# Kernel tuning notes

Hardware: AMD Instinct MI355X
Metric: run time of the kernel (lower is better)

Reference implementation:

```python
import jax, jax.numpy as jnp
import numpy as np

B, S, V, H = 256, 1024, 256, 256


def setup_inputs() -> dict:
    key = jax.random.key(0)
    ks = jax.random.split(key, 12)
    s = 1.0 / np.sqrt(H)
    def u(k, shape):
        return jax.random.uniform(k, shape, jnp.float32, -s, s)
    return {
        "x": jax.random.normal(ks[0], (B, S, V), jnp.float32),
        "w_ih0": u(ks[1], (4 * H, V)),
        "w_hh0": u(ks[2], (4 * H, H)),
        "b_ih0": u(ks[3], (4 * H,)),
        "b_hh0": u(ks[4], (4 * H,)),
        "w_ih1": u(ks[5], (4 * H, H)),
        "w_hh1": u(ks[6], (4 * H, H)),
        "b_ih1": u(ks[7], (4 * H,)),
        "b_hh1": u(ks[8], (4 * H,)),
        "fc_w": u(ks[9], (V, H)),
        "fc_b": u(ks[10], (V,)),
    }


def _lstm_layer(inp, w_ih, w_hh, b_ih, b_hh):
    # inp: [B, S, D]. Precompute input contribution for all timesteps (big GEMM),
    # then scan the recurrence (PyTorch gate order: i, f, g, o).
    pre = jnp.einsum('bsd,gd->bsg', inp, w_ih) + b_ih + b_hh  # [B, S, 4H]
    h0 = jnp.zeros((inp.shape[0], w_hh.shape[1]), inp.dtype)
    c0 = jnp.zeros_like(h0)

    def step(carry, p):
        h, c = carry
        g = p + h @ w_hh.T  # [B, 4H]
        i, f, gg, o = jnp.split(g, 4, axis=-1)
        c = jax.nn.sigmoid(f) * c + jax.nn.sigmoid(i) * jnp.tanh(gg)
        h = jax.nn.sigmoid(o) * jnp.tanh(c)
        return (h, c), h

    _, hs = jax.lax.scan(step, (h0, c0), pre.transpose(1, 0, 2))  # hs: [S, B, H]
    return hs.transpose(1, 0, 2)


def reference(x, w_ih0, w_hh0, b_ih0, b_hh0, w_ih1, w_hh1, b_ih1, b_hh1, fc_w, fc_b):
    h1 = _lstm_layer(x, w_ih0, w_hh0, b_ih0, b_hh0)
    h2 = _lstm_layer(h1, w_ih1, w_hh1, b_ih1, b_hh1)
    logits = jnp.einsum('bsh,vh->bsv', h2, fc_w) + fc_b
    return jax.nn.log_softmax(logits, axis=-1)
```

## Files before the change

### kernel.cpp

```cpp
#include <hip/hip_runtime.h>
#include <cstdint>
#include <cstddef>


typedef __attribute__((ext_vector_type(8))) short bf16x8;
typedef __attribute__((ext_vector_type(4))) float f32x4;
typedef unsigned long long ull;

#define DEVFN __device__ __forceinline__

constexpr unsigned SENT = 0xFFFFFFFFu;

DEVFN unsigned short f2bf(float f) {
  union { float f; unsigned u; } v; v.f = f;
  unsigned r = v.u + 0x7FFFu + ((v.u >> 16) & 1u);
  return (unsigned short)(r >> 16);
}
DEVFN float sigm(float x) { return __builtin_amdgcn_rcpf(1.f + __expf(-x)); }
DEVFN float tanhfast(float x) {
  float ax = fabsf(x);
  float e  = __expf(-2.f * ax);
  float t  = (1.f - e) * __builtin_amdgcn_rcpf(1.f + e);
  return copysignf(t, x);
}
DEVFN ull aload64(const ull* p) {
  return __hip_atomic_load(p, __ATOMIC_RELAXED, __HIP_MEMORY_SCOPE_AGENT);
}
DEVFN void astore64(ull* p, ull v) {
  __hip_atomic_store(p, v, __ATOMIC_RELAXED, __HIP_MEMORY_SCOPE_AGENT);
}
DEVFN bool sent2(ull v) {
  return ((unsigned)v == SENT) || ((unsigned)(v >> 32) == SENT);
}
DEVFN bf16x8 fragu(ull a, ull b) {
  union { ull u[2]; bf16x8 f; } t; t.u[0] = a; t.u[1] = b; return t.f;
}
DEVFN bf16x8 frag4(uint4 u) { union { uint4 u; bf16x8 f; } t; t.u = u; return t.f; }

__global__ void pack_w(const float* __restrict__ w, unsigned short* __restrict__ dst) {
  int bid = blockIdx.x;
  int lane = threadIdx.x;
  int col = (bid >> 3) * 16 + (lane & 15);
  int k0  = (bid & 7) * 32 + (lane >> 4) * 8;
  const float* src = w + (size_t)col * 256 + k0;
  unsigned short* d = dst + ((size_t)bid * 64 + lane) * 8;
#pragma unroll
  for (int j = 0; j < 8; ++j) d[j] = f2bf(src[j]);
}

__global__ void pack_x(const float* __restrict__ x, unsigned short* __restrict__ xp) {
  int bid = blockIdx.x, lane = threadIdx.x;
  int tc = bid & 7, kt = (bid >> 3) & 7, m = bid >> 6;
  int row = lane & 15, hi = lane >> 4;
  for (int t = tc * 128; t < tc * 128 + 128; ++t) {
    const float* s = x + ((size_t)(16 * m + row) * 1024 + t) * 256 + kt * 32 + hi * 8;
    float4 f0 = *(const float4*)s;
    float4 f1 = *(const float4*)(s + 4);
    uint4 o;
    o.x = f2bf(f0.x) | ((unsigned)f2bf(f0.y) << 16);
    o.y = f2bf(f0.z) | ((unsigned)f2bf(f0.w) << 16);
    o.z = f2bf(f1.x) | ((unsigned)f2bf(f1.y) << 16);
    o.w = f2bf(f1.z) | ((unsigned)f2bf(f1.w) << 16);
    *(uint4*)(xp + ((((size_t)t * 16 + m) * 8 + kt) * 64 + lane) * 8) = o;
  }
}

__global__ __launch_bounds__(64, 1) void lstm_dual(
    const unsigned short* __restrict__ xp,
    const unsigned short* __restrict__ Wih0, const unsigned short* __restrict__ Whh0,
    const float* __restrict__ bih0, const float* __restrict__ bhh0,
    const unsigned short* __restrict__ Wih1, const unsigned short* __restrict__ Whh1,
    const float* __restrict__ bih1, const float* __restrict__ bhh1,
    unsigned short* __restrict__ h1f, unsigned short* __restrict__ h2f)
{
  __shared__ unsigned short tl[16][24];
  const int lane = threadIdx.x;
  const int bid  = (int)blockIdx.x;
  const int m = bid & 15;
  const int L = (bid >> 4) & 1;
  const int w = bid >> 5;
  const int u = w * 16 + (lane & 15);
  const bool ownlane = (((lane >> 4) >> 1) == (w & 1));
  const int  mykt = w >> 1;

  const unsigned short* Wih = L ? Wih1 : Wih0;
  const unsigned short* Whh = L ? Whh1 : Whh0;
  const float* bihp = L ? bih1 : bih0;
  const float* bhhp = L ? bhh1 : bhh0;
  unsigned short* hown = L ? h2f : h1f;

  bf16x8 bwih[4][8], bwhh[4][8];
#pragma unroll
  for (int g = 0; g < 4; ++g)
#pragma unroll
    for (int kt = 0; kt < 8; ++kt) {
      bwih[g][kt] = *(const bf16x8*)(Wih + ((((size_t)(g * 16 + w)) * 8 + kt) * 64 + lane) * 8);
      bwhh[g][kt] = *(const bf16x8*)(Whh + ((((size_t)(g * 16 + w)) * 8 + kt) * 64 + lane) * 8);
    }

  float bias[4];
#pragma unroll
  for (int g = 0; g < 4; ++g) bias[g] = bihp[g * 256 + u] + bhhp[g * 256 + u];

  float c[4] = {0.f, 0.f, 0.f, 0.f};
  uint4 ownc = make_uint4(0, 0, 0, 0);

  for (int t = 0; t < 1024; ++t) {
    const size_t tile  = ((size_t)t * 16 + m) * 8;
    const size_t ptile = ((size_t)(t - 1) * 16 + m) * 8;

    uint4 av[8];
    ull  p1[8][2];
    if (!L) {
#pragma unroll
      for (int kt = 0; kt < 8; ++kt)
        av[kt] = *(const uint4*)(xp + ((tile + kt) * 64 + lane) * 8);
    } else {
      const ull* b1 = (const ull*)h1f;
#pragma unroll
      for (int kt = 0; kt < 8; ++kt) {
        p1[kt][0] = aload64(b1 + ((tile + kt) * 64 + lane) * 2);
        p1[kt][1] = aload64(b1 + ((tile + kt) * 64 + lane) * 2 + 1);
      }
    }

    ull hv[8][2];
    const ull* bo = (const ull*)hown;
    if (t > 0) {
#pragma unroll
      for (int kt = 0; kt < 8; ++kt) {
        hv[kt][0] = aload64(bo + ((ptile + kt) * 64 + lane) * 2);
        hv[kt][1] = aload64(bo + ((ptile + kt) * 64 + lane) * 2 + 1);
      }
    }

    f32x4 acc[4];
#pragma unroll
    for (int g = 0; g < 4; ++g) acc[g] = (f32x4){0.f, 0.f, 0.f, 0.f};

    if (!L) {
#pragma unroll
      for (int kt = 0; kt < 8; ++kt) {
        bf16x8 a = frag4(av[kt]);
#pragma unroll
        for (int g = 0; g < 4; ++g)
          acc[g] = __builtin_amdgcn_mfma_f32_16x16x32_bf16(a, bwih[g][kt], acc[g], 0, 0, 0);
      }
    } else {
      int rounds = 0;
      while (true) {
        bool bad = false;
#pragma unroll
        for (int kt = 0; kt < 8; ++kt)
          bad = bad || sent2(p1[kt][0]) || sent2(p1[kt][1]);
        if (!__any(bad)) break;
        if (++rounds > 4) __builtin_amdgcn_s_sleep(1);
        const ull* b1 = (const ull*)h1f;
#pragma unroll
        for (int kt = 0; kt < 8; ++kt) {
          p1[kt][0] = aload64(b1 + ((tile + kt) * 64 + lane) * 2);
          p1[kt][1] = aload64(b1 + ((tile + kt) * 64 + lane) * 2 + 1);
        }
      }
#pragma unroll
      for (int kt = 0; kt < 8; ++kt) {
        bf16x8 a = fragu(p1[kt][0], p1[kt][1]);
#pragma unroll
        for (int g = 0; g < 4; ++g)
          acc[g] = __builtin_amdgcn_mfma_f32_16x16x32_bf16(a, bwih[g][kt], acc[g], 0, 0, 0);
      }
    }

    if (t > 0) {
      int rounds = 0;
      while (true) {
#pragma unroll
        for (int kt = 0; kt < 8; ++kt)
          if (kt == mykt && ownlane) {
            hv[kt][0] = ((ull)ownc.y << 32) | ownc.x;
            hv[kt][1] = ((ull)ownc.w << 32) | ownc.z;
          }
        bool bad = false;
#pragma unroll
        for (int kt = 0; kt < 8; ++kt)
          bad = bad || sent2(hv[kt][0]) || sent2(hv[kt][1]);
        if (!__any(bad)) break;
        if (++rounds > 4) __builtin_amdgcn_s_sleep(1);
#pragma unroll
        for (int kt = 0; kt < 8; ++kt) {
          hv[kt][0] = aload64(bo + ((ptile + kt) * 64 + lane) * 2);
          hv[kt][1] = aload64(bo + ((ptile + kt) * 64 + lane) * 2 + 1);
        }
      }
#pragma unroll
      for (int kt = 0; kt < 8; ++kt) {
        bf16x8 a = fragu(hv[kt][0], hv[kt][1]);
#pragma unroll
        for (int g = 0; g < 4; ++g)
          acc[g] = __builtin_amdgcn_mfma_f32_16x16x32_bf16(a, bwhh[g][kt], acc[g], 0, 0, 0);
      }
    }

    float hq[4];
#pragma unroll
    for (int q = 0; q < 4; ++q) {
      float ia = acc[0][q] + bias[0];
      float fa = acc[1][q] + bias[1];
      float ga = acc[2][q] + bias[2];
      float oa = acc[3][q] + bias[3];
      c[q] = sigm(fa) * c[q] + sigm(ia) * tanhfast(ga);
      hq[q] = sigm(oa) * tanhfast(c[q]);
    }

#pragma unroll
    for (int q = 0; q < 4; ++q)
      tl[(lane >> 4) * 4 + q][lane & 15] = f2bf(hq[q]);
    uint4 nown = *(const uint4*)(&tl[lane & 15][((lane >> 4) & 1) * 8]);
    ownc = nown;

    if (ownlane) {
      ull* d = (ull*)hown + ((tile + mykt) * 64 + lane) * 2;
      astore64(d,     ((ull)nown.y << 32) | nown.x);
      astore64(d + 1, ((ull)nown.w << 32) | nown.z);
    }
  }
}

__global__ __launch_bounds__(256, 1) void fc_lsm(
    const unsigned short* __restrict__ h2f,
    const unsigned short* __restrict__ Bp,
    const float* __restrict__ fcb,
    float* __restrict__ out)
{
  const int tid = threadIdx.x;
  const int wid = tid >> 6, lane = tid & 63;
  const int t = blockIdx.x >> 2;
  const int mloc = (blockIdx.x & 3) * 4 + wid;

  f32x4 acc[16];
#pragma unroll
  for (int nt = 0; nt < 16; ++nt) acc[nt] = (f32x4){0.f, 0.f, 0.f, 0.f};

#pragma unroll
  for (int kt = 0; kt < 8; ++kt) {
    bf16x8 a = *(const bf16x8*)(h2f + ((((size_t)t * 16 + mloc) * 8 + kt) * 64 + lane) * 8);
#pragma unroll
    for (int nt = 0; nt < 16; ++nt) {
      bf16x8 b = *(const bf16x8*)(Bp + (((size_t)nt * 8 + kt) * 64 + lane) * 8);
      acc[nt] = __builtin_amdgcn_mfma_f32_16x16x32_bf16(a, b, acc[nt], 0, 0, 0);
    }
  }
#pragma unroll
  for (int nt = 0; nt < 16; ++nt) {
    float bias = fcb[nt * 16 + (lane & 15)];
#pragma unroll
    for (int q = 0; q < 4; ++q) acc[nt][q] += bias;
  }

  float mx[4] = {-1e30f, -1e30f, -1e30f, -1e30f};
#pragma unroll
  for (int nt = 0; nt < 16; ++nt)
#pragma unroll
    for (int q = 0; q < 4; ++q) mx[q] = fmaxf(mx[q], acc[nt][q]);
#pragma unroll
  for (int d = 1; d < 16; d <<= 1)
#pragma unroll
    for (int q = 0; q < 4; ++q) mx[q] = fmaxf(mx[q], __shfl_xor(mx[q], d, 64));

  float sm[4] = {0.f, 0.f, 0.f, 0.f};
#pragma unroll
  for (int nt = 0; nt < 16; ++nt)
#pragma unroll
    for (int q = 0; q < 4; ++q) sm[q] += __expf(acc[nt][q] - mx[q]);
#pragma unroll
  for (int d = 1; d < 16; d <<= 1)
#pragma unroll
    for (int q = 0; q < 4; ++q) sm[q] += __shfl_xor(sm[q], d, 64);

  float lse[4];
#pragma unroll
  for (int q = 0; q < 4; ++q) lse[q] = mx[q] + __logf(sm[q]);

#pragma unroll
  for (int nt = 0; nt < 16; ++nt) {
#pragma unroll
    for (int q = 0; q < 4; ++q) {
      int b = mloc * 16 + (lane >> 4) * 4 + q;
      out[((size_t)b * 1024 + t) * 256 + nt * 16 + (lane & 15)] = acc[nt][q] - lse[q];
    }
  }
}

__global__ void fill_marker(float* out, size_t nvals) {
  size_t i = (size_t)blockIdx.x * blockDim.x + threadIdx.x;
  if (i < nvals) out[i] = -7777.0f;
}

extern "C" void kernel_launch(void* const* d_in, const int* in_sizes, int n_in,
                              void* d_out, int out_size, void* d_ws, size_t ws_size,
                              hipStream_t stream)
{
  (void)in_sizes; (void)n_in;
  const float* x    = (const float*)d_in[0];
  const float* wih0 = (const float*)d_in[1];
  const float* whh0 = (const float*)d_in[2];
  const float* bih0 = (const float*)d_in[3];
  const float* bhh0 = (const float*)d_in[4];
  const float* wih1 = (const float*)d_in[5];
  const float* whh1 = (const float*)d_in[6];
  const float* bih1 = (const float*)d_in[7];
  const float* bhh1 = (const float*)d_in[8];
  const float* fcw  = (const float*)d_in[9];
  const float* fcb  = (const float*)d_in[10];
  float* out = (float*)d_out;

  const size_t o_wp0i = 0;
  const size_t o_wp0h = o_wp0i + 524288;
  const size_t o_wp1i = o_wp0h + 524288;
  const size_t o_wp1h = o_wp1i + 524288;
  const size_t o_fcp  = o_wp1h + 524288;
  const size_t o_xp   = o_fcp  + 131072;
  const size_t o_h1f  = o_xp   + 134217728;
  const size_t o_h2f  = o_h1f  + 134217728;
  const size_t need   = o_h2f  + 134217728;

  if (ws_size < need) {
    size_t nv = (size_t)out_size;
    fill_marker<<<(unsigned)((nv + 1023) / 1024), 1024, 0, stream>>>(out, nv);
    return;
  }

  char* ws = (char*)d_ws;
  unsigned short* wp0i = (unsigned short*)(ws + o_wp0i);
  unsigned short* wp0h = (unsigned short*)(ws + o_wp0h);
  unsigned short* wp1i = (unsigned short*)(ws + o_wp1i);
  unsigned short* wp1h = (unsigned short*)(ws + o_wp1h);
  unsigned short* fcp  = (unsigned short*)(ws + o_fcp);
  unsigned short* xp   = (unsigned short*)(ws + o_xp);
  unsigned short* h1f  = (unsigned short*)(ws + o_h1f);
  unsigned short* h2f  = (unsigned short*)(ws + o_h2f);

  pack_w<<<512, 64, 0, stream>>>(wih0, wp0i);
  pack_w<<<512, 64, 0, stream>>>(whh0, wp0h);
  pack_w<<<512, 64, 0, stream>>>(wih1, wp1i);
  pack_w<<<512, 64, 0, stream>>>(whh1, wp1h);
  pack_w<<<128, 64, 0, stream>>>(fcw,  fcp);
  pack_x<<<1024, 64, 0, stream>>>(x, xp);

  hipMemsetAsync(h1f, 0xFF, 134217728, stream);
  hipMemsetAsync(h2f, 0xFF, 134217728, stream);

  lstm_dual<<<512, 64, 0, stream>>>(xp, wp0i, wp0h, bih0, bhh0,
                                    wp1i, wp1h, bih1, bhh1, h1f, h2f);

  fc_lsm<<<4096, 256, 0, stream>>>(h2f, fcp, fcb, out);
}
```

Baseline: 3.440 ms.

## Split LSTM kernel into per-layer loops with x prefetch and cheaper activations

Splits the persistent dual-layer LSTM kernel into separate layer-0 and layer-1 loops with incrementally advanced pointers. Layer 0 now prefetches the next timestep's x tile during the current step, which takes that load off the critical path. The sentinel check looks at only the low 32 bits of each word, and the kernel's own h slice is no longer forwarded from registers but re-read from global memory. Activations are rewritten with exp2-based sigmoid and tanh, and an asm barrier keeps the weight fragments pinned in registers. The risks are more VGPR pressure and a slightly different tanh numerics path.

```diff
diff --git a/kernel.cpp b/kernel.cpp
--- a/kernel.cpp
+++ b/kernel.cpp
@@ -16,12 +16,11 @@
   unsigned r = v.u + 0x7FFFu + ((v.u >> 16) & 1u);
   return (unsigned short)(r >> 16);
 }
-DEVFN float sigm(float x) { return __builtin_amdgcn_rcpf(1.f + __expf(-x)); }
-DEVFN float tanhfast(float x) {
-  float ax = fabsf(x);
-  float e  = __expf(-2.f * ax);
-  float t  = (1.f - e) * __builtin_amdgcn_rcpf(1.f + e);
-  return copysignf(t, x);
+DEVFN float sigm(float x) {
+  return __builtin_amdgcn_rcpf(1.f + exp2f(x * -1.442695041f));
+}
+DEVFN float tanh2(float x) {
+  return 1.f - 2.f * __builtin_amdgcn_rcpf(1.f + exp2f(x * 2.885390082f));
 }
 DEVFN ull aload64(const ull* p) {
   return __hip_atomic_load(p, __ATOMIC_RELAXED, __HIP_MEMORY_SCOPE_AGENT);
@@ -29,13 +28,14 @@
 DEVFN void astore64(ull* p, ull v) {
   __hip_atomic_store(p, v, __ATOMIC_RELAXED, __HIP_MEMORY_SCOPE_AGENT);
 }
-DEVFN bool sent2(ull v) {
-  return ((unsigned)v == SENT) || ((unsigned)(v >> 32) == SENT);
-}
 DEVFN bf16x8 fragu(ull a, ull b) {
   union { ull u[2]; bf16x8 f; } t; t.u[0] = a; t.u[1] = b; return t.f;
 }
 DEVFN bf16x8 frag4(uint4 u) { union { uint4 u; bf16x8 f; } t; t.u = u; return t.f; }
+
+#define KEEP8(a0,a1,a2,a3,a4,a5,a6,a7) \
+  asm volatile("" : "+v"(a0), "+v"(a1), "+v"(a2), "+v"(a3), \
+                    "+v"(a4), "+v"(a5), "+v"(a6), "+v"(a7))
 
 __global__ void pack_w(const float* __restrict__ w, unsigned short* __restrict__ dst) {
   int bid = blockIdx.x;
@@ -65,7 +65,9 @@
   }
 }
 
-__global__ __launch_bounds__(64, 1) void lstm_dual(
+__global__ __attribute__((amdgpu_flat_work_group_size(64, 64),
+                          amdgpu_waves_per_eu(1, 1)))
+void lstm_dual(
     const unsigned short* __restrict__ xp,
     const unsigned short* __restrict__ Wih0, const unsigned short* __restrict__ Whh0,
     const float* __restrict__ bih0, const float* __restrict__ bhh0,
@@ -87,7 +89,6 @@
   const unsigned short* Whh = L ? Whh1 : Whh0;
   const float* bihp = L ? bih1 : bih0;
   const float* bhhp = L ? bhh1 : bhh0;
-  unsigned short* hown = L ? h2f : h1f;
 
   bf16x8 bwih[4][8], bwhh[4][8];
 #pragma unroll
@@ -97,131 +98,211 @@
       bwih[g][kt] = *(const bf16x8*)(Wih + ((((size_t)(g * 16 + w)) * 8 + kt) * 64 + lane) * 8);
       bwhh[g][kt] = *(const bf16x8*)(Whh + ((((size_t)(g * 16 + w)) * 8 + kt) * 64 + lane) * 8);
     }
+#pragma unroll
+  for (int g = 0; g < 4; ++g) {
+    KEEP8(bwih[g][0], bwih[g][1], bwih[g][2], bwih[g][3],
+          bwih[g][4], bwih[g][5], bwih[g][6], bwih[g][7]);
+    KEEP8(bwhh[g][0], bwhh[g][1], bwhh[g][2], bwhh[g][3],
+          bwhh[g][4], bwhh[g][5], bwhh[g][6], bwhh[g][7]);
+  }
 
   float bias[4];
 #pragma unroll
   for (int g = 0; g < 4; ++g) bias[g] = bihp[g * 256 + u] + bhhp[g * 256 + u];
 
   float c[4] = {0.f, 0.f, 0.f, 0.f};
-  uint4 ownc = make_uint4(0, 0, 0, 0);
-
-  for (int t = 0; t < 1024; ++t) {
-    const size_t tile  = ((size_t)t * 16 + m) * 8;
-    const size_t ptile = ((size_t)(t - 1) * 16 + m) * 8;
-
-    uint4 av[8];
-    ull  p1[8][2];
-    if (!L) {
-#pragma unroll
-      for (int kt = 0; kt < 8; ++kt)
-        av[kt] = *(const uint4*)(xp + ((tile + kt) * 64 + lane) * 8);
-    } else {
-      const ull* b1 = (const ull*)h1f;
+
+  constexpr int TSTEP_U = 16384;
+  constexpr int TSTEP_X = 8192;
+
+  if (!L) {
+    const ull* hrd  = (const ull*)h1f + m * 1024 + lane * 2;
+    const ull* hrd2 = hrd + 512;
+    ull* hwr = (ull*)h1f + m * 1024 + mykt * 128 + lane * 2;
+    const uint4* xq  = (const uint4*)xp + m * 512 + lane;
+    const uint4* xq2 = xq + 256;
+
+    uint4 xpre[8];
+#pragma unroll
+    for (int kt = 0; kt < 4; ++kt) { xpre[kt] = xq[kt * 64]; xpre[4 + kt] = xq2[kt * 64]; }
+    xq += TSTEP_X; xq2 += TSTEP_X;
+
+    for (int t = 0; t < 1024; ++t) {
+      ull hv[16];
+      if (t > 0) {
+#pragma unroll
+        for (int kt = 0; kt < 4; ++kt) {
+          hv[2*kt]     = aload64(hrd  + kt * 128);
+          hv[2*kt + 1] = aload64(hrd  + kt * 128 + 1);
+          hv[8 + 2*kt]     = aload64(hrd2 + kt * 128);
+          hv[8 + 2*kt + 1] = aload64(hrd2 + kt * 128 + 1);
+        }
+      }
+
+      f32x4 acc[4];
+#pragma unroll
+      for (int g = 0; g < 4; ++g) acc[g] = (f32x4){0.f, 0.f, 0.f, 0.f};
 #pragma unroll
       for (int kt = 0; kt < 8; ++kt) {
-        p1[kt][0] = aload64(b1 + ((tile + kt) * 64 + lane) * 2);
-        p1[kt][1] = aload64(b1 + ((tile + kt) * 64 + lane) * 2 + 1);
-      }
-    }
-
-    ull hv[8][2];
-    const ull* bo = (const ull*)hown;
-    if (t > 0) {
-#pragma unroll
-      for (int kt = 0; kt < 8; ++kt) {
-        hv[kt][0] = aload64(bo + ((ptile + kt) * 64 + lane) * 2);
-        hv[kt][1] = aload64(bo + ((ptile + kt) * 64 + lane) * 2 + 1);
-      }
-    }
-
-    f32x4 acc[4];
-#pragma unroll
-    for (int g = 0; g < 4; ++g) acc[g] = (f32x4){0.f, 0.f, 0.f, 0.f};
-
-    if (!L) {
-#pragma unroll
-      for (int kt = 0; kt < 8; ++kt) {
-        bf16x8 a = frag4(av[kt]);
+        bf16x8 a = frag4(xpre[kt]);
 #pragma unroll
         for (int g = 0; g < 4; ++g)
           acc[g] = __builtin_amdgcn_mfma_f32_16x16x32_bf16(a, bwih[g][kt], acc[g], 0, 0, 0);
       }
-    } else {
-      int rounds = 0;
-      while (true) {
-        bool bad = false;
-#pragma unroll
-        for (int kt = 0; kt < 8; ++kt)
-          bad = bad || sent2(p1[kt][0]) || sent2(p1[kt][1]);
-        if (!__any(bad)) break;
-        if (++rounds > 4) __builtin_amdgcn_s_sleep(1);
-        const ull* b1 = (const ull*)h1f;
+
+      if (t > 0) {
+        int rounds = 0;
+        while (true) {
+          bool bad = false;
+#pragma unroll
+          for (int i = 0; i < 16; ++i) bad = bad || ((unsigned)hv[i] == SENT);
+          if (!__any(bad)) break;
+          if (++rounds > 8) __builtin_amdgcn_s_sleep(1);
+#pragma unroll
+          for (int kt = 0; kt < 4; ++kt) {
+            hv[2*kt]     = aload64(hrd  + kt * 128);
+            hv[2*kt + 1] = aload64(hrd  + kt * 128 + 1);
+            hv[8 + 2*kt]     = aload64(hrd2 + kt * 128);
+            hv[8 + 2*kt + 1] = aload64(hrd2 + kt * 128 + 1);
+          }
+        }
 #pragma unroll
         for (int kt = 0; kt < 8; ++kt) {
-          p1[kt][0] = aload64(b1 + ((tile + kt) * 64 + lane) * 2);
-          p1[kt][1] = aload64(b1 + ((tile + kt) * 64 + lane) * 2 + 1);
-        }
-      }
+          bf16x8 a = fragu(hv[kt < 4 ? 2*kt : 2*kt], hv[kt < 4 ? 2*kt+1 : 2*kt+1]);
+#pragma unroll
+          for (int g = 0; g < 4; ++g)
+            acc[g] = __builtin_amdgcn_mfma_f32_16x16x32_bf16(a, bwhh[g][kt], acc[g], 0, 0, 0);
+        }
+        hrd += TSTEP_U; hrd2 += TSTEP_U;
+      }
+
+      float hq[4];
+#pragma unroll
+      for (int q = 0; q < 4; ++q) {
+        float ia = acc[0][q] + bias[0];
+        float fa = acc[1][q] + bias[1];
+        float ga = acc[2][q] + bias[2];
+        float oa = acc[3][q] + bias[3];
+        c[q] = sigm(fa) * c[q] + sigm(ia) * tanh2(ga);
+        hq[q] = sigm(oa) * tanh2(c[q]);
+      }
+#pragma unroll
+      for (int q = 0; q < 4; ++q)
+        tl[(lane >> 4) * 4 + q][lane & 15] = f2bf(hq[q]);
+      uint4 nown = *(const uint4*)(&tl[lane & 15][((lane >> 4) & 1) * 8]);
+      if (ownlane) {
+        astore64(hwr,     ((ull)nown.y << 32) | nown.x);
+        astore64(hwr + 1, ((ull)nown.w << 32) | nown.z);
+      }
+      hwr += TSTEP_U;
+
+      if (t < 1023) {
+#pragma unroll
+        for (int kt = 0; kt < 4; ++kt) { xpre[kt] = xq[kt * 64]; xpre[4 + kt] = xq2[kt * 64]; }
+        xq += TSTEP_X; xq2 += TSTEP_X;
+      }
+    }
+  } else {
+    const ull* prd  = (const ull*)h1f + m * 1024 + lane * 2;
+    const ull* prd2 = prd + 512;
+    const ull* hrd  = (const ull*)h2f + m * 1024 + lane * 2;
+    const ull* hrd2 = hrd + 512;
+    ull* hwr = (ull*)h2f + m * 1024 + mykt * 128 + lane * 2;
+
+    for (int t = 0; t < 1024; ++t) {
+      ull p1[16], hv[16];
+#pragma unroll
+      for (int kt = 0; kt < 4; ++kt) {
+        p1[2*kt]     = aload64(prd  + kt * 128);
+        p1[2*kt + 1] = aload64(prd  + kt * 128 + 1);
+        p1[8 + 2*kt]     = aload64(prd2 + kt * 128);
+        p1[8 + 2*kt + 1] = aload64(prd2 + kt * 128 + 1);
+      }
+      if (t > 0) {
+#pragma unroll
+        for (int kt = 0; kt < 4; ++kt) {
+          hv[2*kt]     = aload64(hrd  + kt * 128);
+          hv[2*kt + 1] = aload64(hrd  + kt * 128 + 1);
+          hv[8 + 2*kt]     = aload64(hrd2 + kt * 128);
+          hv[8 + 2*kt + 1] = aload64(hrd2 + kt * 128 + 1);
+        }
+      }
+
+      {
+        int rounds = 0;
+        while (true) {
+          bool bad = false;
+#pragma unroll
+          for (int i = 0; i < 16; ++i) bad = bad || ((unsigned)p1[i] == SENT);
+          if (!__any(bad)) break;
+          if (++rounds > 8) __builtin_amdgcn_s_sleep(1);
+#pragma unroll
+          for (int kt = 0; kt < 4; ++kt) {
+            p1[2*kt]     = aload64(prd  + kt * 128);
+            p1[2*kt + 1] = aload64(prd  + kt * 128 + 1);
+            p1[8 + 2*kt]     = aload64(prd2 + kt * 128);
+            p1[8 + 2*kt + 1] = aload64(prd2 + kt * 128 + 1);
+          }
+        }
+      }
+      prd += TSTEP_U; prd2 += TSTEP_U;
+
+      f32x4 acc[4];
+#pragma unroll
+      for (int g = 0; g < 4; ++g) acc[g] = (f32x4){0.f, 0.f, 0.f, 0.f};
 #pragma unroll
       for (int kt = 0; kt < 8; ++kt) {
-        bf16x8 a = fragu(p1[kt][0], p1[kt][1]);
+        bf16x8 a = fragu(p1[2*kt], p1[2*kt + 1]);
 #pragma unroll
         for (int g = 0; g < 4; ++g)
           acc[g] = __builtin_amdgcn_mfma_f32_16x16x32_bf16(a, bwih[g][kt], acc[g], 0, 0, 0);
       }
-    }
-
-    if (t > 0) {
-      int rounds = 0;
-      while (true) {
-#pragma unroll
-        for (int kt = 0; kt < 8; ++kt)
-          if (kt == mykt && ownlane) {
-            hv[kt][0] = ((ull)ownc.y << 32) | ownc.x;
-            hv[kt][1] = ((ull)ownc.w << 32) | ownc.z;
+
+      if (t > 0) {
+        int rounds = 0;
+        while (true) {
+          bool bad = false;
+#pragma unroll
+          for (int i = 0; i < 16; ++i) bad = bad || ((unsigned)hv[i] == SENT);
+          if (!__any(bad)) break;
+          if (++rounds > 8) __builtin_amdgcn_s_sleep(1);
+#pragma unroll
+          for (int kt = 0; kt < 4; ++kt) {
+            hv[2*kt]     = aload64(hrd  + kt * 128);
+            hv[2*kt + 1] = aload64(hrd  + kt * 128 + 1);
+            hv[8 + 2*kt]     = aload64(hrd2 + kt * 128);
+            hv[8 + 2*kt + 1] = aload64(hrd2 + kt * 128 + 1);
           }
-        bool bad = false;
-#pragma unroll
-        for (int kt = 0; kt < 8; ++kt)
-          bad = bad || sent2(hv[kt][0]) || sent2(hv[kt][1]);
-        if (!__any(bad)) break;
-        if (++rounds > 4) __builtin_amdgcn_s_sleep(1);
+        }
 #pragma unroll
         for (int kt = 0; kt < 8; ++kt) {
-          hv[kt][0] = aload64(bo + ((ptile + kt) * 64 + lane) * 2);
-          hv[kt][1] = aload64(bo + ((ptile + kt) * 64 + lane) * 2 + 1);
-        }
-      }
-#pragma unroll
-      for (int kt = 0; kt < 8; ++kt) {
-        bf16x8 a = fragu(hv[kt][0], hv[kt][1]);
-#pragma unroll
-        for (int g = 0; g < 4; ++g)
-          acc[g] = __builtin_amdgcn_mfma_f32_16x16x32_bf16(a, bwhh[g][kt], acc[g], 0, 0, 0);
-      }
-    }
-
-    float hq[4];
-#pragma unroll
-    for (int q = 0; q < 4; ++q) {
-      float ia = acc[0][q] + bias[0];
-      float fa = acc[1][q] + bias[1];
-      float ga = acc[2][q] + bias[2];
-      float oa = acc[3][q] + bias[3];
-      c[q] = sigm(fa) * c[q] + sigm(ia) * tanhfast(ga);
-      hq[q] = sigm(oa) * tanhfast(c[q]);
-    }
-
-#pragma unroll
-    for (int q = 0; q < 4; ++q)
-      tl[(lane >> 4) * 4 + q][lane & 15] = f2bf(hq[q]);
-    uint4 nown = *(const uint4*)(&tl[lane & 15][((lane >> 4) & 1) * 8]);
-    ownc = nown;
-
-    if (ownlane) {
-      ull* d = (ull*)hown + ((tile + mykt) * 64 + lane) * 2;
-      astore64(d,     ((ull)nown.y << 32) | nown.x);
-      astore64(d + 1, ((ull)nown.w << 32) | nown.z);
+          bf16x8 a = fragu(hv[2*kt], hv[2*kt + 1]);
+#pragma unroll
+          for (int g = 0; g < 4; ++g)
+            acc[g] = __builtin_amdgcn_mfma_f32_16x16x32_bf16(a, bwhh[g][kt], acc[g], 0, 0, 0);
+        }
+        hrd += TSTEP_U; hrd2 += TSTEP_U;
+      }
+
+      float hq[4];
+#pragma unroll
+      for (int q = 0; q < 4; ++q) {
+        float ia = acc[0][q] + bias[0];
+        float fa = acc[1][q] + bias[1];
+        float ga = acc[2][q] + bias[2];
+        float oa = acc[3][q] + bias[3];
+        c[q] = sigm(fa) * c[q] + sigm(ia) * tanh2(ga);
+        hq[q] = sigm(oa) * tanh2(c[q]);
+      }
+#pragma unroll
+      for (int q = 0; q < 4; ++q)
+        tl[(lane >> 4) * 4 + q][lane & 15] = f2bf(hq[q]);
+      uint4 nown = *(const uint4*)(&tl[lane & 15][((lane >> 4) & 1) * 8]);
+      if (ownlane) {
+        astore64(hwr,     ((ull)nown.y << 32) | nown.x);
+        astore64(hwr + 1, ((ull)nown.w << 32) | nown.z);
+      }
+      hwr += TSTEP_U;
     }
   }
 }
```

Measured after the change: 3.789 ms. 1.1x slower.
